# Performance work log

Measured on AMD Instinct MI355X. Metric: run time of the kernel, lower is better.

## Reference

```python
import jax, jax.numpy as jnp
import numpy as np
from jax import lax

# ---- constants matching init_kwargs ----
NY, NX = 1024, 1024
DX, DY = 50.0, 50.0
TTOT = 32.0
DTMAX = 0.5
RHO, G, FD = 910.0, 9.81, 1e-17
EPS = 1e-10
T_FREQ = 5.0
N_STEPS = 64            # fixed step count (>= TTOT/DTMAX); dt masked to 0 once time >= TTOT
LAPSE = 0.0065          # degC per m elevation lapse rate (SMB model)
MELT_FACTOR = 0.5       # m ice / (degC * yr) ablation factor (SMB model)


def update_smb(Z_surf, precip, T_ma_lowest, T_mj_lowest, ice_mask):
    # Lapse-rate temperatures at the surface
    T_ma = T_ma_lowest - LAPSE * Z_surf   # mean annual temperature
    T_mj = T_mj_lowest - LAPSE * Z_surf   # mean July temperature
    accumulation = precip * (T_ma < 0.0).astype(Z_surf.dtype)
    ablation = MELT_FACTOR * jnp.maximum(T_mj, 0.0)
    return (accumulation - ablation) * ice_mask


def setup_inputs() -> dict:
    key = jax.random.key(0)
    k1, k2, k3 = jax.random.split(key, 3)
    # smooth mountain topography: 2500 m gaussian massif + small noise
    y = np.arange(NY, dtype=np.float32) * DY
    x = np.arange(NX, dtype=np.float32) * DX
    yy, xx = np.meshgrid(y, x, indexing="ij")
    cy, cx = y.mean(), x.mean()
    sigma = 0.25 * NX * DX
    z = 2500.0 * np.exp(-((yy - cy) ** 2 + (xx - cx) ** 2) / (2.0 * sigma ** 2))
    Z_topo = jnp.asarray(z, dtype=jnp.float32) + 5.0 * jax.random.normal(k1, (NY, NX), dtype=jnp.float32)
    precip_tensor = 2.0 * jax.random.uniform(k2, (NY, NX), dtype=jnp.float32)  # m ice / yr
    T_ma_lowest = jnp.float32(8.0) + jax.random.normal(k3, (), dtype=jnp.float32)
    T_mj_lowest = T_ma_lowest + jnp.float32(8.0)
    ice_mask = jnp.ones((NY, NX), dtype=jnp.float32)
    return {"precip_tensor": precip_tensor, "T_ma_lowest": T_ma_lowest,
            "T_mj_lowest": T_mj_lowest, "Z_topo": Z_topo, "ice_mask": ice_mask}


def _glacier_step(carry, _, Z_topo, precip, T_ma_lowest, T_mj_lowest, ice_mask):
    H_ice, Z_surf, smb, time, t_last = carry
    # staggered-grid averages and slopes (SIA diffusion)
    H_avg = 0.25 * (H_ice[:-1, :-1] + H_ice[1:, 1:] + H_ice[:-1, 1:] + H_ice[1:, :-1])
    Sx = (Z_surf[:, 1:] - Z_surf[:, :-1]) / DX
    Sy = (Z_surf[1:, :] - Z_surf[:-1, :]) / DY
    Sx = 0.5 * (Sx[:-1, :] + Sx[1:, :])          # (NY-1, NX-1)
    Sy = 0.5 * (Sy[:, :-1] + Sy[:, 1:])          # (NY-1, NX-1)
    Snorm = jnp.sqrt(Sx ** 2 + Sy ** 2 + EPS)
    D = FD * (RHO * G) ** 3 * H_avg ** 5 * Snorm ** 2 + EPS
    # adaptive CFL dt; torch uses .item() so dt is a non-differentiable constant
    dt = jnp.minimum(min(DX, DY) ** 2 / (2.7 * jnp.max(D)), DTMAX)
    dt = lax.stop_gradient(dt)
    dt = jnp.where(time < TTOT, dt, 0.0)         # freeze once ttot is reached
    qx = -(0.5 * (D[:-1, :] + D[1:, :])) * (Z_surf[1:-1, 1:] - Z_surf[1:-1, :-1]) / DX
    qy = -(0.5 * (D[:, :-1] + D[:, 1:])) * (Z_surf[1:, 1:-1] - Z_surf[:-1, 1:-1]) / DY
    dHdt = -(jnp.diff(qx, axis=1) / DX + jnp.diff(qy, axis=0) / DY)  # (NY-2, NX-2)
    H_new = H_ice.at[1:-1, 1:-1].add(dt * (dHdt + smb[1:-1, 1:-1]))
    H_new = jnp.maximum(H_new, 0.0)
    Z_new = Z_topo + H_new
    time = time + dt
    # refresh SMB every T_FREQ model years
    do_upd = (time - t_last) >= T_FREQ
    smb_new = update_smb(Z_new, precip, T_ma_lowest, T_mj_lowest, ice_mask)
    smb = jnp.where(do_upd, smb_new, smb)
    t_last = jnp.where(do_upd, time, t_last)
    return (H_new, Z_new, smb, time, t_last), None


def reference(precip_tensor, T_ma_lowest, T_mj_lowest, Z_topo, ice_mask):
    H_ice = jnp.zeros((NY, NX), dtype=jnp.float32)
    Z_surf = Z_topo + H_ice
    smb = update_smb(Z_surf, precip_tensor, T_ma_lowest, T_mj_lowest, ice_mask)
    time = jnp.float32(0.0)
    t_last = jnp.float32(0.0)
    step = lambda c, x: _glacier_step(c, x, Z_topo, precip_tensor, T_ma_lowest, T_mj_lowest, ice_mask)
    (H_ice, _, _, _, _), _ = lax.scan(step, (H_ice, Z_surf, smb, time, t_last), None, length=N_STEPS)
    return H_ice
```

## Files before the change

kernel.cpp:

```cpp
#include <hip/hip_runtime.h>
#include <math.h>

#define NYg 1024
#define NXg 1024
#define W   1024
#define NSTEPS 64
#define NBLK 256
#define EN (NBLK * W)

#define SLOT_STRIDE 32
#define SLOT_GROUP  256
#define NSLOTG      (NSTEPS + 1)
#define WS_CNT  (NSLOTG * SLOT_GROUP)
#define WS_NBF  (WS_CNT + 8 * 32)
#define WS_CTRL_END (WS_NBF + 256 * 32)
#define WS_GRIDS 32768

constexpr float DXf   = 50.0f;
constexpr float DYf   = 50.0f;
constexpr float TTOTf = 32.0f;
constexpr float DTMAXf= 0.5f;
constexpr float EPSf  = 1e-10f;
constexpr float TFREQ = 5.0f;
constexpr float LAPSE = 0.0065f;
constexpr float MELTF = 0.5f;
constexpr double RHOG = 910.0 * 9.81;
constexpr float  CDf  = (float)(1e-17 * RHOG * RHOG * RHOG);

__device__ __forceinline__ float scloadf(const float* p) {
    return __hip_atomic_load(p, __ATOMIC_RELAXED, __HIP_MEMORY_SCOPE_SYSTEM);
}
__device__ __forceinline__ void scstoref(float* p, float v) {
    __hip_atomic_store(p, v, __ATOMIC_RELAXED, __HIP_MEMORY_SCOPE_SYSTEM);
}
__device__ __forceinline__ unsigned scloadu(const unsigned* p) {
    return __hip_atomic_load(p, __ATOMIC_RELAXED, __HIP_MEMORY_SCOPE_SYSTEM);
}

__device__ __forceinline__ float dfunc(float h00, float h01, float h10, float h11,
                                       float z00, float z01, float z10, float z11)
{
    float havg = 0.25f * (h00 + h11 + h01 + h10);
    float sx = ((z01 - z00) + (z11 - z10)) * (0.5f / DXf);
    float sy = ((z10 - z00) + (z11 - z01)) * (0.5f / DYf);
    float sn = sqrtf(sx * sx + sy * sy + EPSf);
    float h2 = havg * havg;
    float h4 = h2 * h2;
    return CDf * (h4 * havg) * (sn * sn) + EPSf;
}

__global__ __launch_bounds__(256) void k_init(unsigned* __restrict__ ctrl)
{
    int idx = blockIdx.x * blockDim.x + threadIdx.x;
    int stride = gridDim.x * blockDim.x;
    for (int i = idx; i < WS_CTRL_END; i += stride) {
        unsigned v = 0u;
        if (i < SLOT_GROUP && (i & (SLOT_STRIDE - 1)) == 0) v = __float_as_uint(EPSf);
        ctrl[i] = v;
    }
}

__global__ __launch_bounds__(1024, 1) void k_run(
    float* __restrict__ EZa0, float* __restrict__ EZa1,
    float* __restrict__ EZb0, float* __restrict__ EZb1,
    float* __restrict__ EDa0, float* __restrict__ EDa1,
    float* __restrict__ EDb0, float* __restrict__ EDb1,
    const float* __restrict__ ztopo, const float* __restrict__ precip,
    const float* __restrict__ mask, const float* __restrict__ tma,
    const float* __restrict__ tmj, unsigned* __restrict__ ctrl,
    float* __restrict__ Hout)
{
    __shared__ float sZ[5][W];
    __shared__ float sH[5][W];
    __shared__ float sD[4][W];
    __shared__ float smax16[16];
    __shared__ float sMD;

    unsigned* slots = ctrl;
    unsigned* cnt   = ctrl + WS_CNT;
    unsigned* nbf   = ctrl + WS_NBF;

    const int c   = threadIdx.x;
    const int b   = blockIdx.x;
    const int r0  = b * 4;
    const int grp = b & 7;
    const int lane = c & 63, wid = c >> 6;
    const bool hasA = (b > 0), hasB = (b < NBLK - 1);
    const bool cL = (c >= 1), cR = (c <= NXg - 2);
    const int cm = (c == 0) ? 0 : c - 1;
    const int cp = (c == W - 1) ? W - 1 : c + 1;

    const float TMA = tma[0], TMJ = tmj[0];

    float z_[7];
    float h_[5];
    float dreg[4];
    float dtop, dtopL;
    float dbot, dbotL;
    float smbr[5], ztr[5];

    #pragma unroll
    for (int q = 0; q < 7; ++q) {
        int r = r0 - 1 + q;
        z_[q] = (r >= 0 && r < NYg) ? ztopo[r * W + c] : 0.0f;
    }
    #pragma unroll
    for (int rr = 0; rr < 5; ++rr) {
        int r = r0 + rr;
        h_[rr] = 0.0f;
        if (r < NYg) {
            float z = z_[rr + 1];
            ztr[rr] = z;
            float t_ma = TMA - LAPSE * z;
            float t_mj = TMJ - LAPSE * z;
            float acc  = (t_ma < 0.0f) ? precip[r * W + c] : 0.0f;
            float abl  = MELTF * fmaxf(t_mj, 0.0f);
            smbr[rr] = (acc - abl) * mask[r * W + c];
            sZ[rr][c] = z;
            sH[rr][c] = 0.0f;
        } else {
            ztr[rr] = 0.0f; smbr[rr] = 0.0f;
            sZ[rr][c] = 0.0f;
            sH[rr][c] = 0.0f;
        }
    }
    dtop = EPSf; dtopL = EPSf; dbot = EPSf; dbotL = EPSf;
    #pragma unroll
    for (int q = 0; q < 4; ++q) { dreg[q] = EPSf; sD[q][c] = EPSf; }
    __syncthreads();

    float t = 0.0f, tl = 0.0f;

    for (int s = 0; s < NSTEPS; ++s) {
        const float* EZar = (s & 1) ? EZa1 : EZa0;
        float*       EZaw = (s & 1) ? EZa0 : EZa1;
        const float* EZbr = (s & 1) ? EZb1 : EZb0;
        float*       EZbw = (s & 1) ? EZb0 : EZb1;
        const float* EDar = (s & 1) ? EDa1 : EDa0;
        float*       EDaw = (s & 1) ? EDa0 : EDa1;
        const float* EDbr = (s & 1) ? EDb1 : EDb0;
        float*       EDbw = (s & 1) ? EDb0 : EDb1;

        if (s > 0) {
            if (c == 0 && hasA)
                while (scloadu(&nbf[(b - 1) * 32]) < (unsigned)s) __builtin_amdgcn_s_sleep(1);
            if (c == 64 && hasB)
                while (scloadu(&nbf[(b + 1) * 32]) < (unsigned)s) __builtin_amdgcn_s_sleep(1);
            __syncthreads();
            if (hasA) {
                z_[0] = scloadf(EZbr + (b - 1) * W + c);
                if (cR) dtop  = scloadf(EDbr + (b - 1) * W + c);
                if (cL) dtopL = scloadf(EDbr + (b - 1) * W + (c-1));
            }
            if (hasB) {
                z_[6] = scloadf(EZar + (b + 1) * W + c);
                if (cR) dbot  = scloadf(EDar + (b + 1) * W + c);
                if (cL) dbotL = scloadf(EDar + (b + 1) * W + (c-1));
            }
        }

        float dl[6], doa[6];
        dl[0] = dtopL;      doa[0] = dtop;
        dl[1] = sD[0][cm];  doa[1] = dreg[0];
        dl[2] = sD[1][cm];  doa[2] = dreg[1];
        dl[3] = sD[2][cm];  doa[3] = dreg[2];
        dl[4] = sD[3][cm];  doa[4] = dreg[3];
        dl[5] = dbotL;      doa[5] = dbot;

        float zl[5], zr[5];
        #pragma unroll
        for (int q = 0; q < 5; ++q) { zl[q] = sZ[q][cm]; zr[q] = sZ[q][cp]; }

        float qy[6];
        #pragma unroll
        for (int k = 0; k < 6; ++k)
            qy[k] = -0.5f * (dl[k] + doa[k]) * (z_[k + 1] - z_[k]) * (1.0f / DYf);

        float dh[5];
        bool  inter[5];
        #pragma unroll
        for (int rr = 0; rr < 5; ++rr) {
            int r = r0 + rr;
            bool iv = (r >= 1 && r <= NYg - 2 && cL && cR);
            float zc  = z_[rr + 1];
            float qxR = -0.5f * (doa[rr] + doa[rr + 1]) * (zr[rr] - zc) * (1.0f / DXf);
            float qxL = -0.5f * (dl[rr]  + dl[rr + 1])  * (zc - zl[rr]) * (1.0f / DXf);
            float d = -((qxR - qxL) * (1.0f / DXf) + (qy[rr + 1] - qy[rr]) * (1.0f / DYf));
            dh[rr] = iv ? d : 0.0f;
            inter[rr] = iv;
        }

        if (c < 8) {
            unsigned tgt = 32u * (unsigned)s;
            while (scloadu(&cnt[c * 32]) < tgt) __builtin_amdgcn_s_sleep(1);
            float v = __uint_as_float(scloadu(&slots[s * SLOT_GROUP + c * SLOT_STRIDE]));
            v = fmaxf(v, __shfl_xor(v, 4, 64));
            v = fmaxf(v, __shfl_xor(v, 2, 64));
            v = fmaxf(v, __shfl_xor(v, 1, 64));
            if (c == 0) sMD = v;
        }
        __syncthreads();

        float mD = sMD;
        float dt = fminf(2500.0f / (2.7f * mD), DTMAXf);
        if (!(t < TTOTf)) dt = 0.0f;
        float nt  = t + dt;
        bool  upd = (nt - tl) >= TFREQ;

        #pragma unroll
        for (int rr = 0; rr < 5; ++rr) {
            int r = r0 + rr;
            if (r < NYg) {
                float h, z;
                if (inter[rr]) { h = fmaxf(h_[rr] + dt * (dh[rr] + smbr[rr]), 0.0f);
                                 z = ztr[rr] + h; }
                else           { h = 0.0f; z = z_[rr + 1]; }
                h_[rr] = h; z_[rr + 1] = z;
                sZ[rr][c] = z;
                sH[rr][c] = h;
                if (rr == 1 && hasA) scstoref(EZaw + b * W + c, z);
                if (rr == 3 && hasB) scstoref(EZbw + b * W + c, z);
                if (upd) {
                    float t_ma = TMA - LAPSE * z;
                    float t_mj = TMJ - LAPSE * z;
                    float acc  = (t_ma < 0.0f) ? precip[r * W + c] : 0.0f;
                    float abl  = MELTF * fmaxf(t_mj, 0.0f);
                    smbr[rr] = (acc - abl) * mask[r * W + c];
                }
            } else {
                h_[rr] = 0.0f;
            }
        }
        __syncthreads();

        if (s < NSTEPS - 1) {
            float m = 0.0f;
            float dv[4];
            #pragma unroll
            for (int rr = 0; rr < 4; ++rr) {
                int i = r0 + rr;
                float dd = 0.0f;
                if (i <= NYg - 2 && cR) {
                    dd = dfunc(h_[rr], sH[rr][c + 1],
                               h_[rr + 1], sH[rr + 1][c + 1],
                               z_[rr + 1], sZ[rr][c + 1],
                               z_[rr + 2], sZ[rr + 1][c + 1]);
                    m = fmaxf(m, dd);
                    if (rr == 0 && hasA) scstoref(EDaw + b * W + c, dd);
                    if (rr == 3 && hasB) scstoref(EDbw + b * W + c, dd);
                }
                dv[rr] = dd;
            }
            sD[0][c] = dv[0];
            sD[1][c] = dv[1];
            sD[2][c] = dv[2];
            sD[3][c] = dv[3];
            dreg[0] = dv[0]; dreg[1] = dv[1]; dreg[2] = dv[2]; dreg[3] = dv[3];
            #pragma unroll
            for (int off = 32; off >= 1; off >>= 1)
                m = fmaxf(m, __shfl_xor(m, off, 64));
            if (lane == 0) smax16[wid] = m;
            asm volatile("s_waitcnt vmcnt(0)" ::: "memory");
            __syncthreads();
            if (c == 0) {
                __hip_atomic_store(&nbf[b * 32], (unsigned)(s + 1),
                                   __ATOMIC_RELAXED, __HIP_MEMORY_SCOPE_SYSTEM);
                #pragma unroll
                for (int q = 1; q < 16; ++q) m = fmaxf(m, smax16[q]);
                __hip_atomic_fetch_max(&slots[(s + 1) * SLOT_GROUP + grp * SLOT_STRIDE],
                                       __float_as_uint(m),
                                       __ATOMIC_RELAXED, __HIP_MEMORY_SCOPE_SYSTEM);
                asm volatile("s_waitcnt vmcnt(0)" ::: "memory");
                __hip_atomic_fetch_add(&cnt[grp * 32], 1u,
                                       __ATOMIC_RELAXED, __HIP_MEMORY_SCOPE_SYSTEM);
            }
        }

        t = nt;
        if (upd) tl = nt;
    }

    #pragma unroll
    for (int rr = 0; rr < 4; ++rr)
        Hout[(r0 + rr) * W + c] = h_[rr];
}

extern "C" void kernel_launch(void* const* d_in, const int* in_sizes, int n_in,
                              void* d_out, int out_size, void* d_ws, size_t ws_size,
                              hipStream_t stream)
{
    const float* precip = (const float*)d_in[0];
    const float* tma    = (const float*)d_in[1];
    const float* tmj    = (const float*)d_in[2];
    const float* ztopo  = (const float*)d_in[3];
    const float* mask   = (const float*)d_in[4];

    unsigned* ctrl = (unsigned*)d_ws;
    float* g = (float*)d_ws + WS_GRIDS;
    float* EZa0 = g + 0 * EN; float* EZa1 = g + 1 * EN;
    float* EZb0 = g + 2 * EN; float* EZb1 = g + 3 * EN;
    float* EDa0 = g + 4 * EN; float* EDa1 = g + 5 * EN;
    float* EDb0 = g + 6 * EN; float* EDb1 = g + 7 * EN;

    k_init<<<dim3(64), dim3(256), 0, stream>>>(ctrl);

    k_run<<<dim3(256), dim3(1024), 0, stream>>>(EZa0, EZa1, EZb0, EZb1,
                                                EDa0, EDa1, EDb0, EDb1,
                                                ztopo, precip, mask, tma, tmj,
                                                ctrl, (float*)d_out);
}
```

Before: 419.3 us.

## Replace grouped atomic max/counter barrier with per-block slot flags

Each block now writes its local max diffusivity into its own per-step slot, and 256 threads poll all slots for a nonzero value and reduce them with wave shuffles. This replaces the eight grouped atomic fetch_max counters and fetch_add counters. Neighbor-flag polling is now done by every thread of the block instead of one thread followed by a __syncthreads, removing one block barrier per step. The aim is to cut atomic contention and serialization in the global dt reduction, at the cost of more polling traffic and an extra __syncthreads before publishing the max. Correctness relies on the slots being zero-initialized and every max being nonzero (D is at least EPS).

```diff
diff --git a/kernel.cpp b/kernel.cpp
--- a/kernel.cpp
+++ b/kernel.cpp
@@ -8,12 +8,10 @@
 #define NBLK 256
 #define EN (NBLK * W)
 
-#define SLOT_STRIDE 32
-#define SLOT_GROUP  256
-#define NSLOTG      (NSTEPS + 1)
-#define WS_CNT  (NSLOTG * SLOT_GROUP)
-#define WS_NBF  (WS_CNT + 8 * 32)
-#define WS_CTRL_END (WS_NBF + 256 * 32)
+#define WS_SLOTS 0
+#define NSLOTW   ((NSTEPS + 1) * NBLK)
+#define WS_NBF   24576
+#define WS_CTRL_END 32768
 #define WS_GRIDS 32768
 
 constexpr float DXf   = 50.0f;
@@ -55,7 +53,7 @@
     int stride = gridDim.x * blockDim.x;
     for (int i = idx; i < WS_CTRL_END; i += stride) {
         unsigned v = 0u;
-        if (i < SLOT_GROUP && (i & (SLOT_STRIDE - 1)) == 0) v = __float_as_uint(EPSf);
+        if (i < NBLK) v = __float_as_uint(EPSf);
         ctrl[i] = v;
     }
 }
@@ -74,16 +72,14 @@
     __shared__ float sH[5][W];
     __shared__ float sD[4][W];
     __shared__ float smax16[16];
-    __shared__ float sMD;
-
-    unsigned* slots = ctrl;
-    unsigned* cnt   = ctrl + WS_CNT;
-    unsigned* nbf   = ctrl + WS_NBF;
+    __shared__ float smax4[4];
+
+    float*    slotsf = (float*)ctrl + WS_SLOTS;
+    unsigned* nbf    = ctrl + WS_NBF;
 
     const int c   = threadIdx.x;
     const int b   = blockIdx.x;
     const int r0  = b * 4;
-    const int grp = b & 7;
     const int lane = c & 63, wid = c >> 6;
     const bool hasA = (b > 0), hasB = (b < NBLK - 1);
     const bool cL = (c >= 1), cR = (c <= NXg - 2);
@@ -142,11 +138,10 @@
         float*       EDbw = (s & 1) ? EDb0 : EDb1;
 
         if (s > 0) {
-            if (c == 0 && hasA)
+            if (hasA)
                 while (scloadu(&nbf[(b - 1) * 32]) < (unsigned)s) __builtin_amdgcn_s_sleep(1);
-            if (c == 64 && hasB)
+            if (hasB)
                 while (scloadu(&nbf[(b + 1) * 32]) < (unsigned)s) __builtin_amdgcn_s_sleep(1);
-            __syncthreads();
             if (hasA) {
                 z_[0] = scloadf(EZbr + (b - 1) * W + c);
                 if (cR) dtop  = scloadf(EDbr + (b - 1) * W + c);
@@ -190,18 +185,18 @@
             inter[rr] = iv;
         }
 
-        if (c < 8) {
-            unsigned tgt = 32u * (unsigned)s;
-            while (scloadu(&cnt[c * 32]) < tgt) __builtin_amdgcn_s_sleep(1);
-            float v = __uint_as_float(scloadu(&slots[s * SLOT_GROUP + c * SLOT_STRIDE]));
-            v = fmaxf(v, __shfl_xor(v, 4, 64));
-            v = fmaxf(v, __shfl_xor(v, 2, 64));
-            v = fmaxf(v, __shfl_xor(v, 1, 64));
-            if (c == 0) sMD = v;
+        if (c < NBLK) {
+            const float* sl = slotsf + s * NBLK + c;
+            float v = scloadf(sl);
+            while (__float_as_uint(v) == 0u) { __builtin_amdgcn_s_sleep(1); v = scloadf(sl); }
+            #pragma unroll
+            for (int off = 32; off >= 1; off >>= 1)
+                v = fmaxf(v, __shfl_xor(v, off, 64));
+            if (lane == 0) smax4[wid] = v;
         }
         __syncthreads();
 
-        float mD = sMD;
+        float mD = fmaxf(fmaxf(smax4[0], smax4[1]), fmaxf(smax4[2], smax4[3]));
         float dt = fminf(2500.0f / (2.7f * mD), DTMAXf);
         if (!(t < TTOTf)) dt = 0.0f;
         float nt  = t + dt;
@@ -260,20 +255,17 @@
             for (int off = 32; off >= 1; off >>= 1)
                 m = fmaxf(m, __shfl_xor(m, off, 64));
             if (lane == 0) smax16[wid] = m;
+            __syncthreads();
+            if (c == 0) {
+                #pragma unroll
+                for (int q = 1; q < 16; ++q) m = fmaxf(m, smax16[q]);
+                scstoref(slotsf + (s + 1) * NBLK + b, m);
+            }
             asm volatile("s_waitcnt vmcnt(0)" ::: "memory");
             __syncthreads();
-            if (c == 0) {
+            if (c == 0)
                 __hip_atomic_store(&nbf[b * 32], (unsigned)(s + 1),
                                    __ATOMIC_RELAXED, __HIP_MEMORY_SCOPE_SYSTEM);
-                #pragma unroll
-                for (int q = 1; q < 16; ++q) m = fmaxf(m, smax16[q]);
-                __hip_atomic_fetch_max(&slots[(s + 1) * SLOT_GROUP + grp * SLOT_STRIDE],
-                                       __float_as_uint(m),
-                                       __ATOMIC_RELAXED, __HIP_MEMORY_SCOPE_SYSTEM);
-                asm volatile("s_waitcnt vmcnt(0)" ::: "memory");
-                __hip_atomic_fetch_add(&cnt[grp * 32], 1u,
-                                       __ATOMIC_RELAXED, __HIP_MEMORY_SCOPE_SYSTEM);
-            }
         }
 
         t = nt;
```

Result: faster. 393.5 us (-6.1%).
